# Kernel tuning notes

Measured on AMD Instinct MI355X. Metric: run time of the kernel, lower is better.

## Reference

```python
import jax, jax.numpy as jnp
import numpy as np

B, T, E, H = 4, 1024, 1024, 16
HS = E // H  # 64
EPS = 1e-5


def layernorm(x, g, b):
    mu = jnp.mean(x, axis=-1, keepdims=True)
    var = jnp.mean((x - mu) ** 2, axis=-1, keepdims=True)
    return (x - mu) * jax.lax.rsqrt(var + EPS) * g + b


def setup_inputs() -> dict:
    key = jax.random.key(0)
    ks = jax.random.split(key, 10)
    s = 0.02
    return {
        "v": jax.random.normal(ks[0], (B, T, E), jnp.float32),
        "k": jax.random.normal(ks[1], (B, T, E), jnp.float32),
        "q": jax.random.normal(ks[2], (B, T, E), jnp.float32),
        "ln_g": jnp.ones((E,), jnp.float32),
        "ln_b": jnp.zeros((E,), jnp.float32),
        # per-head projection weights stacked: [E, H, HS] (x @ W form)
        "Wq": jax.random.normal(ks[3], (E, H, HS), jnp.float32) * s,
        "Wk": jax.random.normal(ks[4], (E, H, HS), jnp.float32) * s,
        "Wv": jax.random.normal(ks[5], (E, H, HS), jnp.float32) * s,
        "Wp": jax.random.normal(ks[6], (E, E), jnp.float32) * s,
        "bp": jnp.zeros((E,), jnp.float32),
    }


def reference(v, k, q, ln_g, ln_b, Wq, Wk, Wv, Wp, bp):
    # shared LayerNorm applied to all three streams
    vn = layernorm(v, ln_g, ln_b)
    kn = layernorm(k, ln_g, ln_b)
    qn = layernorm(q, ln_g, ln_b)
    # batched per-head projections: [B,T,E] x [E,H,HS] -> [B,H,T,HS]
    qh = jnp.einsum("bte,ehd->bhtd", qn, Wq)
    kh = jnp.einsum("bte,ehd->bhtd", kn, Wk)
    vh = jnp.einsum("bte,ehd->bhtd", vn, Wv)
    # NOTE: original scales by C^-0.5 where C = embedding_dim (not head_size)
    scale = jnp.float32(E) ** -0.5
    scores = jnp.einsum("bhtd,bhsd->bhts", qh, kh) * scale  # [B,H,T,T]
    causal = jnp.tril(jnp.ones((T, T), bool))
    scores = jnp.where(causal, scores, jnp.finfo(scores.dtype).min)
    w = jax.nn.softmax(scores, axis=-1)
    out = jnp.einsum("bhts,bhsd->bhtd", w, vh)  # [B,H,T,HS]
    out = out.transpose(0, 2, 1, 3).reshape(B, T, E)  # concat heads
    return out @ Wp + bp
```

## Files before the change

kernel.cpp:

```cpp
#include <hip/hip_runtime.h>
#include <stdint.h>

#define B_ 4
#define T_ 1024
#define E_ 1024
#define H_ 16
#define HS_ 64
#define BT_ 4096

typedef unsigned short u16;
typedef __attribute__((ext_vector_type(8))) short bf16x8;
typedef __attribute__((ext_vector_type(4))) float f32x4;

__device__ __forceinline__ u16 f2bf(float f) {
    unsigned u = __float_as_uint(f);
    u += 0x7fff + ((u >> 16) & 1);
    return (u16)(u >> 16);
}

__device__ __forceinline__ u16 f2bf_fast(float f) {
    return (u16)((__float_as_uint(f) + 0x8000u) >> 16);
}

__device__ __forceinline__ float fexp2(float x) {
#if __has_builtin(__builtin_amdgcn_exp2f)
    return __builtin_amdgcn_exp2f(x);
#else
    float r; asm("v_exp_f32 %0, %1" : "=v"(r) : "v"(x)); return r;
#endif
}

__device__ __forceinline__ float frcp(float x) {
#if __has_builtin(__builtin_amdgcn_rcpf)
    return __builtin_amdgcn_rcpf(x);
#else
    float r; asm("v_rcp_f32 %0, %1" : "=v"(r) : "v"(x)); return r;
#endif
}

__device__ __forceinline__ void gll16(const void* g, void* l) {
    __builtin_amdgcn_global_load_lds(
        (const __attribute__((address_space(1))) unsigned int*)g,
        (__attribute__((address_space(3))) unsigned int*)l, 16, 0, 0);
}

__global__ __launch_bounds__(256) void ln_all(
    const float* __restrict__ v, const float* __restrict__ k,
    const float* __restrict__ q, const float* __restrict__ g,
    const float* __restrict__ b,
    u16* __restrict__ vn, u16* __restrict__ kn, u16* __restrict__ qn)
{
    int row = blockIdx.x;
    int which = row >> 12;
    int r = row & 4095;
    const float* src = which == 0 ? v : which == 1 ? k : q;
    u16* dst = which == 0 ? vn : which == 1 ? kn : qn;

    int t = threadIdx.x;
    float4 x = ((const float4*)(src + (size_t)r * E_))[t];
    float s  = x.x + x.y + x.z + x.w;
    float ss = x.x * x.x + x.y * x.y + x.z * x.z + x.w * x.w;
    for (int off = 32; off; off >>= 1) {
        s  += __shfl_down(s, off, 64);
        ss += __shfl_down(ss, off, 64);
    }
    __shared__ float red[8];
    int w = t >> 6, l = t & 63;
    if (l == 0) { red[w] = s; red[4 + w] = ss; }
    __syncthreads();
    float fs  = red[0] + red[1] + red[2] + red[3];
    float fss = red[4] + red[5] + red[6] + red[7];
    float mu  = fs * (1.0f / E_);
    float var = fss * (1.0f / E_) - mu * mu;
    float rstd = rsqrtf(var + 1e-5f);

    float4 gg = ((const float4*)g)[t];
    float4 bb = ((const float4*)b)[t];
    ushort4 o;
    o.x = f2bf((x.x - mu) * rstd * gg.x + bb.x);
    o.y = f2bf((x.y - mu) * rstd * gg.y + bb.y);
    o.z = f2bf((x.z - mu) * rstd * gg.z + bb.z);
    o.w = f2bf((x.w - mu) * rstd * gg.w + bb.w);
    ((ushort4*)(dst + (size_t)r * E_))[t] = o;
}

__global__ __launch_bounds__(256) void wcast_t(
    const float* __restrict__ wq, const float* __restrict__ wk,
    const float* __restrict__ wv, const float* __restrict__ wp,
    u16* __restrict__ tq, u16* __restrict__ tk,
    u16* __restrict__ tv, u16* __restrict__ tp)
{
    int z = blockIdx.z;
    const float* src = z == 0 ? wq : z == 1 ? wk : z == 2 ? wv : wp;
    u16* dst = z == 0 ? tq : z == 1 ? tk : z == 2 ? tv : tp;
    __shared__ float tile[32][33];
    int n0 = blockIdx.x * 32, k0 = blockIdx.y * 32;
    int tx = threadIdx.x & 31, ty = threadIdx.x >> 5;
    for (int i = 0; i < 4; i++)
        tile[ty + i * 8][tx] = src[(size_t)(k0 + ty + i * 8) * E_ + n0 + tx];
    __syncthreads();
    for (int i = 0; i < 4; i++)
        dst[(size_t)(n0 + ty + i * 8) * E_ + k0 + tx] = f2bf(tile[tx][ty + i * 8]);
}

__global__ __launch_bounds__(512, 2) void gemm8ph(
    const u16* __restrict__ Xall, const u16* __restrict__ Wall,
    u16* __restrict__ qh, u16* __restrict__ kh, u16* __restrict__ vt)
{
    __shared__ __attribute__((aligned(16))) u16 lds[2][2][256 * 64];

    int lid = blockIdx.x + 4 * blockIdx.y;
    int swz = (lid & 7) * 24 + (lid >> 3);
    int bx = swz & 3, by = swz >> 2;
    int z  = by >> 4;

    int t = threadIdx.x, w = t >> 6, l = t & 63;
    int lr = l & 15, lg = l >> 4;
    int wm = w >> 2, wn = w & 3;
    int ris = l >> 3;
    int csw = (l & 7) ^ ris;
    int swk = lr & 7;

    const char* Xb = (const char*)Xall + (size_t)by * 256 * 2048;
    const char* Wb = (const char*)Wall + ((size_t)z * 1024 + (size_t)bx * 256) * 2048;

    f32x4 acc[8][4];
    f32x4 zero = {0.f, 0.f, 0.f, 0.f};
    #pragma unroll
    for (int i = 0; i < 8; i++)
        #pragma unroll
        for (int j = 0; j < 4; j++) acc[i][j] = zero;

    auto stage = [&](int kt, int g, int buf) {
        int s = w * 4 + g;
        size_t rowoff = (size_t)(s * 8 + ris) * 2048;
        int koff = kt * 128 + csw * 16;
        gll16(Xb + rowoff + koff, (char*)&lds[buf][0][s * 512] + l * 16);
        gll16(Wb + rowoff + koff, (char*)&lds[buf][1][s * 512] + l * 16);
    };

    for (int g = 0; g < 4; g++) stage(0, g, 0);

    const int NT = 16;
    for (int kt = 0; kt < NT; kt++) {
        int cur = kt & 1, nxt = cur ^ 1;
        bool pre = (kt + 1 < NT);

        if (pre) {
            stage(kt + 1, 0, nxt);
            asm volatile("s_waitcnt vmcnt(2)" ::: "memory");
        } else {
            asm volatile("s_waitcnt vmcnt(0)" ::: "memory");
        }
        __builtin_amdgcn_s_barrier();
        asm volatile("" ::: "memory");

        const u16* As = &lds[cur][0][0];
        const u16* Bs = &lds[cur][1][0];

        bf16x8 bfr[4][2];
        #pragma unroll
        for (int nf = 0; nf < 4; nf++)
            #pragma unroll
            for (int kk = 0; kk < 2; kk++)
                bfr[nf][kk] = *(const bf16x8*)
                    &Bs[(wn * 64 + nf * 16 + lr) * 64 + ((kk * 4 + lg) ^ swk) * 8];

        #pragma unroll
        for (int g = 0; g < 4; g++) {
            if (g && pre) stage(kt + 1, g, nxt);
            bf16x8 af[2][2];
            #pragma unroll
            for (int i = 0; i < 2; i++)
                #pragma unroll
                for (int kk = 0; kk < 2; kk++)
                    af[i][kk] = *(const bf16x8*)
                        &As[(wm * 128 + (g * 2 + i) * 16 + lr) * 64 +
                            ((kk * 4 + lg) ^ swk) * 8];
            __builtin_amdgcn_s_setprio(1);
            #pragma unroll
            for (int i = 0; i < 2; i++)
                #pragma unroll
                for (int nf = 0; nf < 4; nf++)
                    #pragma unroll
                    for (int kk = 0; kk < 2; kk++)
                        acc[g * 2 + i][nf] = __builtin_amdgcn_mfma_f32_16x16x32_bf16(
                            af[i][kk], bfr[nf][kk], acc[g * 2 + i][nf], 0, 0, 0);
            __builtin_amdgcn_s_setprio(0);
        }
        asm volatile("" ::: "memory");
        __builtin_amdgcn_s_barrier();
    }

    if (z < 2) {
        u16* outB = z == 0 ? qh : kh;
        float sc = z == 0 ? 0.04508422f : 1.0f;
        #pragma unroll
        for (int mg = 0; mg < 8; mg++)
            #pragma unroll
            for (int nf = 0; nf < 4; nf++)
                #pragma unroll
                for (int r = 0; r < 4; r++) {
                    int mrow = (by & 15) * 256 + wm * 128 + mg * 16 + lg * 4 + r;
                    int col  = bx * 256 + wn * 64 + nf * 16 + lr;
                    int bb = mrow >> 10, tt = mrow & 1023;
                    int hh = col >> 6, dd = col & 63;
                    outB[(((size_t)(bb * H_ + hh)) * T_ + tt) * HS_ + dd] =
                        f2bf(acc[mg][nf][r] * sc);
                }
    } else {
        __syncthreads();
        u16* Tt = &lds[0][0][0] + w * 4608;
        int hh = bx * 4 + wn;
        u16* outV = vt + ((size_t)(((by & 15) * 256 + wm * 128) >> 10) * H_ + hh)
                         * HS_ * T_;
        #pragma unroll
        for (int half = 0; half < 2; half++) {
            #pragma unroll
            for (int mg2 = 0; mg2 < 4; mg2++)
                #pragma unroll
                for (int nf = 0; nf < 4; nf++)
                    #pragma unroll
                    for (int r = 0; r < 4; r++)
                        Tt[(nf * 16 + lr) * 72 + mg2 * 16 + lg * 4 + r] =
                            f2bf(acc[half * 4 + mg2][nf][r]);
            int mbase = (by & 15) * 256 + wm * 128 + half * 64;
            int tbase = mbase & 1023;
            int dl = l >> 3, tc = l & 7;
            #pragma unroll
            for (int u = 0; u < 8; u++) {
                int d = u * 8 + dl;
                bf16x8 vv = *(const bf16x8*)&Tt[d * 72 + tc * 8];
                *(bf16x8*)&outV[(size_t)d * T_ + tbase + tc * 8] = vv;
            }
        }
    }
}

__global__ __launch_bounds__(256) void gemm128(
    const u16* __restrict__ X, const u16* __restrict__ Wt,
    float* __restrict__ outF, const float* __restrict__ bias)
{
    __shared__ __attribute__((aligned(16))) char smem[32768];
    int lid = blockIdx.x + 8 * blockIdx.y;
    int swz = (lid & 7) * 32 + (lid >> 3);
    int bx = swz & 7;
    int by = swz >> 3;

    const int K = 1024;
    int n0 = bx * 128, m0 = by * 128;
    int t = threadIdx.x, w = t >> 6, l = t & 63;
    int lr = l & 15, lg = l >> 4, wm = w >> 1, wn = w & 1;

    f32x4 acc[4][4];
    f32x4 zero = {0.f, 0.f, 0.f, 0.f};
    for (int i = 0; i < 4; i++)
        for (int j = 0; j < 4; j++) acc[i][j] = zero;

    const char* Xb = (const char*)X + (size_t)m0 * 2048;
    const char* Wb = (const char*)Wt + (size_t)n0 * 2048;

    int scol = ((l & 3) ^ ((l >> 3) & 3)) * 16;

    auto stage = [&](int k0, int buf) {
        int kb = k0 * 2;
        for (int j = 0; j < 2; j++) {
            int seg = w * 2 + j;
            int row = seg * 16 + (l >> 2);
            gll16(Xb + (size_t)row * 2048 + kb + scol,
                  smem + buf * 8192 + seg * 1024 + l * 16);
            gll16(Wb + (size_t)row * 2048 + kb + scol,
                  smem + 16384 + buf * 8192 + seg * 1024 + l * 16);
        }
    };

    stage(0, 0);
    __syncthreads();
    int b = 0;
    int swr = (lr >> 1) & 3;
    for (int k0 = 0; k0 < K; k0 += 32) {
        if (k0 + 32 < K) stage(k0 + 32, b ^ 1);
        const u16* As = (const u16*)(smem + b * 8192);
        const u16* Bs = (const u16*)(smem + 16384 + b * 8192);
        bf16x8 af[4], bfr[4];
        for (int i = 0; i < 4; i++)
            af[i] = *(const bf16x8*)&As[(wm * 64 + i * 16 + lr) * 32 + (lg ^ swr) * 8];
        for (int j = 0; j < 4; j++)
            bfr[j] = *(const bf16x8*)&Bs[(wn * 64 + j * 16 + lr) * 32 + (lg ^ swr) * 8];
        for (int i = 0; i < 4; i++)
            for (int j = 0; j < 4; j++)
                acc[i][j] = __builtin_amdgcn_mfma_f32_16x16x32_bf16(
                    af[i], bfr[j], acc[i][j], 0, 0, 0);
        __syncthreads();
        b ^= 1;
    }

    for (int i = 0; i < 4; i++)
        for (int j = 0; j < 4; j++)
            for (int r = 0; r < 4; r++) {
                int row = m0 + wm * 64 + i * 16 + lg * 4 + r;
                int col = n0 + wn * 64 + j * 16 + lr;
                outF[(size_t)row * E_ + col] = acc[i][j][r] + bias[col];
            }
}

__global__ __launch_bounds__(256) void attn(
    const u16* __restrict__ Qh, const u16* __restrict__ Kh,
    const u16* __restrict__ Vt, u16* __restrict__ Out)
{
    int lid = blockIdx.x + 8 * blockIdx.y;
    int swz = (lid & 7) * 64 + (lid >> 3);
    int qt = 7 - (swz & 7);
    int bh = swz >> 3;
    int b = bh >> 4, h = bh & 15;
    int t = threadIdx.x, w = t >> 6, l = t & 63;
    int lr = l & 15, lg = l >> 4;
    int sw = lr & 7;

    __shared__ __attribute__((aligned(16))) u16 Ks[2][4096];
    __shared__ __attribute__((aligned(16))) u16 Vs[2][4096];
    __shared__ __attribute__((aligned(16))) u16 Ps[4][2048];

    const char* Kb = (const char*)(Kh + (size_t)bh * T_ * HS_);
    const char* Vb = (const char*)(Vt + (size_t)bh * HS_ * T_);
    const u16*  Qb = Qh + (size_t)bh * T_ * HS_;

    int ris = l >> 3;
    int csw = (l & 7) ^ ris;

    bf16x8 qf[2][2];
    for (int i = 0; i < 2; i++) {
        int qrow = qt * 128 + w * 32 + i * 16 + lr;
        qf[i][0] = *(const bf16x8*)&Qb[qrow * 64 + lg * 8];
        qf[i][1] = *(const bf16x8*)&Qb[qrow * 64 + 32 + lg * 8];
    }

    f32x4 zero = {0.f, 0.f, 0.f, 0.f};
    f32x4 o[2][4];
    float m[2][4], psum[2][4];
    for (int i = 0; i < 2; i++)
        for (int nf = 0; nf < 4; nf++) o[i][nf] = zero;
    for (int i = 0; i < 2; i++)
        for (int r = 0; r < 4; r++) { m[i][r] = -1e30f; psum[i][r] = 0.f; }

    int nkv = 2 * qt + 2;

    auto stageKV = [&](int kt2, int bsel) {
        int kv0 = kt2 * 64;
        for (int j = 0; j < 2; j++) {
            int seg = w * 2 + j;
            int row = seg * 8 + ris;
            gll16(Kb + (size_t)(kv0 + row) * 128 + csw * 16,
                  (char*)Ks[bsel] + seg * 1024);
            gll16(Vb + (size_t)row * 2048 + (size_t)kv0 * 2 + csw * 16,
                  (char*)Vs[bsel] + seg * 1024);
        }
    };

    stageKV(0, 0);
    __syncthreads();
    int bsel = 0;

    for (int kt = 0; kt < nkv; kt++) {
        if (kt + 1 < nkv) stageKV(kt + 1, bsel ^ 1);

        int kv0 = kt * 64;
        const u16* Kl = Ks[bsel];
        const u16* Vl = Vs[bsel];

        f32x4 s[2][4];
        __builtin_amdgcn_s_setprio(1);
        for (int kf = 0; kf < 4; kf++) {
            int key = kf * 16 + lr;
            bf16x8 bk0 = *(const bf16x8*)&Kl[key * 64 + (lg ^ sw) * 8];
            bf16x8 bk1 = *(const bf16x8*)&Kl[key * 64 + ((lg + 4) ^ sw) * 8];
            for (int i = 0; i < 2; i++) {
                s[i][kf] = __builtin_amdgcn_mfma_f32_16x16x32_bf16(qf[i][0], bk0, zero, 0, 0, 0);
                s[i][kf] = __builtin_amdgcn_mfma_f32_16x16x32_bf16(qf[i][1], bk1, s[i][kf], 0, 0, 0);
            }
        }
        __builtin_amdgcn_s_setprio(0);

        if (kt >= 2 * qt) {
            for (int i = 0; i < 2; i++)
                for (int kf = 0; kf < 4; kf++)
                    for (int r = 0; r < 4; r++) {
                        int key = kv0 + kf * 16 + lr;
                        int qr  = qt * 128 + w * 32 + i * 16 + lg * 4 + r;
                        if (key > qr) s[i][kf][r] = -1e30f;
                    }
        }

        float pmr[2][4];
        bool ok = true;
        for (int i = 0; i < 2; i++)
            for (int r = 0; r < 4; r++) {
                pmr[i][r] = fmaxf(fmaxf(s[i][0][r], s[i][1][r]),
                                  fmaxf(s[i][2][r], s[i][3][r]));
                ok &= (pmr[i][r] <= m[i][r] + 11.5f);
            }
        if (!__all(ok)) {
            for (int i = 0; i < 2; i++)
                for (int r = 0; r < 4; r++) {
                    float mt = pmr[i][r];
                    for (int off = 1; off < 16; off <<= 1)
                        mt = fmaxf(mt, __shfl_xor(mt, off, 64));
                    float mn = fmaxf(m[i][r], mt);
                    float al = fexp2(m[i][r] - mn);
                    m[i][r] = mn;
                    psum[i][r] *= al;
                    for (int nf = 0; nf < 4; nf++) o[i][nf][r] *= al;
                }
        }

        for (int i = 0; i < 2; i++)
            for (int kf = 0; kf < 4; kf++)
                for (int r = 0; r < 4; r++) {
                    float p = fexp2(s[i][kf][r] - m[i][r]);
                    psum[i][r] += p;
                    int row = i * 16 + lg * 4 + r;
                    int ch  = (kf * 2 + (lr >> 3)) ^ (row & 7);
                    Ps[w][row * 64 + ch * 8 + sw] = f2bf_fast(p);
                }

        __builtin_amdgcn_s_setprio(1);
        for (int ks = 0; ks < 2; ks++) {
            bf16x8 pa0 = *(const bf16x8*)&Ps[w][(lr) * 64 + ((ks * 4 + lg) ^ sw) * 8];
            bf16x8 pa1 = *(const bf16x8*)&Ps[w][(16 + lr) * 64 + ((ks * 4 + lg) ^ sw) * 8];
            for (int nf = 0; nf < 4; nf++) {
                int d = nf * 16 + lr;
                bf16x8 bv = *(const bf16x8*)&Vl[d * 64 + ((ks * 4 + lg) ^ sw) * 8];
                o[0][nf] = __builtin_amdgcn_mfma_f32_16x16x32_bf16(pa0, bv, o[0][nf], 0, 0, 0);
                o[1][nf] = __builtin_amdgcn_mfma_f32_16x16x32_bf16(pa1, bv, o[1][nf], 0, 0, 0);
            }
        }
        __builtin_amdgcn_s_setprio(0);
        __syncthreads();
        bsel ^= 1;
    }

    for (int i = 0; i < 2; i++)
        for (int r = 0; r < 4; r++) {
            for (int off = 1; off < 16; off <<= 1)
                psum[i][r] += __shfl_xor(psum[i][r], off, 64);
            psum[i][r] = frcp(psum[i][r]);
        }

    for (int i = 0; i < 2; i++)
        for (int nf = 0; nf < 4; nf++)
            for (int r = 0; r < 4; r++) {
                int row = qt * 128 + w * 32 + i * 16 + lg * 4 + r;
                int col = h * 64 + nf * 16 + lr;
                Out[((size_t)(b * T_ + row)) * E_ + col] = f2bf(o[i][nf][r] * psum[i][r]);
            }
}

extern "C" void kernel_launch(void* const* d_in, const int* in_sizes, int n_in,
                              void* d_out, int out_size, void* d_ws, size_t ws_size,
                              hipStream_t stream) {
    const float* v  = (const float*)d_in[0];
    const float* k  = (const float*)d_in[1];
    const float* q  = (const float*)d_in[2];
    const float* g  = (const float*)d_in[3];
    const float* be = (const float*)d_in[4];
    const float* Wq = (const float*)d_in[5];
    const float* Wk = (const float*)d_in[6];
    const float* Wv = (const float*)d_in[7];
    const float* Wp = (const float*)d_in[8];
    const float* bp = (const float*)d_in[9];
    float* out = (float*)d_out;

    char* ws = (char*)d_ws;
    u16* qh  = (u16*)(ws);
    u16* kh  = (u16*)(ws + (8u  << 20));
    u16* vt  = (u16*)(ws + (16u << 20));
    u16* qn  = (u16*)(ws + (24u << 20));
    u16* kn  = (u16*)(ws + (32u << 20));
    u16* vn  = (u16*)(ws + (40u << 20));
    u16* wtq = (u16*)(ws + (48u << 20));
    u16* wtk = (u16*)(ws + (50u << 20));
    u16* wtv = (u16*)(ws + (52u << 20));
    u16* wtp = (u16*)(ws + (54u << 20));
    u16* ao  = (u16*)(ws + (24u << 20));

    hipLaunchKernelGGL(wcast_t, dim3(32, 32, 4), dim3(256), 0, stream,
                       Wq, Wk, Wv, Wp, wtq, wtk, wtv, wtp);
    hipLaunchKernelGGL(ln_all, dim3(3 * BT_), dim3(256), 0, stream,
                       v, k, q, g, be, vn, kn, qn);
    hipLaunchKernelGGL(gemm8ph, dim3(4, 48), dim3(512), 0, stream,
                       qn, wtq, qh, kh, vt);
    hipLaunchKernelGGL(attn, dim3(8, 64), dim3(256), 0, stream,
                       qh, kh, vt, ao);
    hipLaunchKernelGGL(gemm128, dim3(8, 32), dim3(256), 0, stream,
                       ao, wtp, out, bp);
}
```

Before: 202.8 us.

## Split attention tile across 8 waves and compute row sums via MFMA

The attention kernel now launches 512 threads (8 waves) per 128-query block, with each wave owning 16 query rows instead of 32. This halves per-wave registers and gives more waves to hide latency. The softmax denominator is now computed with an extra MFMA against a ones vector using the bf16-rounded probabilities, which replaces the scalar psum accumulation and the final cross-lane shuffle reduction. In exchange, each wave makes fewer MFMAs per LDS load of K and V fragments, and the per-block shared-memory staging is split across more waves.

Measured after the change: 198.2 us. 2.3% less time.

```diff
diff --git a/kernel.cpp b/kernel.cpp
--- a/kernel.cpp
+++ b/kernel.cpp
@@ -304,7 +304,7 @@
             }
 }
 
-__global__ __launch_bounds__(256) void attn(
+__global__ __launch_bounds__(512, 4) void attn(
     const u16* __restrict__ Qh, const u16* __restrict__ Kh,
     const u16* __restrict__ Vt, u16* __restrict__ Out)
 {
@@ -319,7 +319,7 @@
 
     __shared__ __attribute__((aligned(16))) u16 Ks[2][4096];
     __shared__ __attribute__((aligned(16))) u16 Vs[2][4096];
-    __shared__ __attribute__((aligned(16))) u16 Ps[4][2048];
+    __shared__ __attribute__((aligned(16))) u16 Ps[8][1024];
 
     const char* Kb = (const char*)(Kh + (size_t)bh * T_ * HS_);
     const char* Vb = (const char*)(Vt + (size_t)bh * HS_ * T_);
@@ -328,33 +328,30 @@
     int ris = l >> 3;
     int csw = (l & 7) ^ ris;
 
-    bf16x8 qf[2][2];
-    for (int i = 0; i < 2; i++) {
-        int qrow = qt * 128 + w * 32 + i * 16 + lr;
-        qf[i][0] = *(const bf16x8*)&Qb[qrow * 64 + lg * 8];
-        qf[i][1] = *(const bf16x8*)&Qb[qrow * 64 + 32 + lg * 8];
-    }
+    int qrow = qt * 128 + w * 16 + lr;
+    bf16x8 qf0 = *(const bf16x8*)&Qb[qrow * 64 + lg * 8];
+    bf16x8 qf1 = *(const bf16x8*)&Qb[qrow * 64 + 32 + lg * 8];
+
+    bf16x8 onesb;
+    #pragma unroll
+    for (int j = 0; j < 8; j++) onesb[j] = (short)0x3F80;
 
     f32x4 zero = {0.f, 0.f, 0.f, 0.f};
-    f32x4 o[2][4];
-    float m[2][4], psum[2][4];
-    for (int i = 0; i < 2; i++)
-        for (int nf = 0; nf < 4; nf++) o[i][nf] = zero;
-    for (int i = 0; i < 2; i++)
-        for (int r = 0; r < 4; r++) { m[i][r] = -1e30f; psum[i][r] = 0.f; }
+    f32x4 o[4], ps;
+    float m[4];
+    for (int nf = 0; nf < 4; nf++) o[nf] = zero;
+    ps = zero;
+    for (int r = 0; r < 4; r++) m[r] = -1e30f;
 
     int nkv = 2 * qt + 2;
 
     auto stageKV = [&](int kt2, int bsel) {
         int kv0 = kt2 * 64;
-        for (int j = 0; j < 2; j++) {
-            int seg = w * 2 + j;
-            int row = seg * 8 + ris;
-            gll16(Kb + (size_t)(kv0 + row) * 128 + csw * 16,
-                  (char*)Ks[bsel] + seg * 1024);
-            gll16(Vb + (size_t)row * 2048 + (size_t)kv0 * 2 + csw * 16,
-                  (char*)Vs[bsel] + seg * 1024);
-        }
+        int row = w * 8 + ris;
+        gll16(Kb + (size_t)(kv0 + row) * 128 + csw * 16,
+              (char*)Ks[bsel] + w * 1024);
+        gll16(Vb + (size_t)row * 2048 + (size_t)kv0 * 2 + csw * 16,
+              (char*)Vs[bsel] + w * 1024);
     };
 
     stageKV(0, 0);
@@ -368,70 +365,61 @@
         const u16* Kl = Ks[bsel];
         const u16* Vl = Vs[bsel];
 
-        f32x4 s[2][4];
+        f32x4 s[4];
         __builtin_amdgcn_s_setprio(1);
         for (int kf = 0; kf < 4; kf++) {
             int key = kf * 16 + lr;
             bf16x8 bk0 = *(const bf16x8*)&Kl[key * 64 + (lg ^ sw) * 8];
             bf16x8 bk1 = *(const bf16x8*)&Kl[key * 64 + ((lg + 4) ^ sw) * 8];
-            for (int i = 0; i < 2; i++) {
-                s[i][kf] = __builtin_amdgcn_mfma_f32_16x16x32_bf16(qf[i][0], bk0, zero, 0, 0, 0);
-                s[i][kf] = __builtin_amdgcn_mfma_f32_16x16x32_bf16(qf[i][1], bk1, s[i][kf], 0, 0, 0);
-            }
+            s[kf] = __builtin_amdgcn_mfma_f32_16x16x32_bf16(qf0, bk0, zero, 0, 0, 0);
+            s[kf] = __builtin_amdgcn_mfma_f32_16x16x32_bf16(qf1, bk1, s[kf], 0, 0, 0);
         }
         __builtin_amdgcn_s_setprio(0);
 
         if (kt >= 2 * qt) {
-            for (int i = 0; i < 2; i++)
-                for (int kf = 0; kf < 4; kf++)
-                    for (int r = 0; r < 4; r++) {
-                        int key = kv0 + kf * 16 + lr;
-                        int qr  = qt * 128 + w * 32 + i * 16 + lg * 4 + r;
-                        if (key > qr) s[i][kf][r] = -1e30f;
-                    }
-        }
-
-        float pmr[2][4];
-        bool ok = true;
-        for (int i = 0; i < 2; i++)
-            for (int r = 0; r < 4; r++) {
-                pmr[i][r] = fmaxf(fmaxf(s[i][0][r], s[i][1][r]),
-                                  fmaxf(s[i][2][r], s[i][3][r]));
-                ok &= (pmr[i][r] <= m[i][r] + 11.5f);
-            }
-        if (!__all(ok)) {
-            for (int i = 0; i < 2; i++)
-                for (int r = 0; r < 4; r++) {
-                    float mt = pmr[i][r];
-                    for (int off = 1; off < 16; off <<= 1)
-                        mt = fmaxf(mt, __shfl_xor(mt, off, 64));
-                    float mn = fmaxf(m[i][r], mt);
-                    float al = fexp2(m[i][r] - mn);
-                    m[i][r] = mn;
-                    psum[i][r] *= al;
-                    for (int nf = 0; nf < 4; nf++) o[i][nf][r] *= al;
-                }
-        }
-
-        for (int i = 0; i < 2; i++)
             for (int kf = 0; kf < 4; kf++)
                 for (int r = 0; r < 4; r++) {
-                    float p = fexp2(s[i][kf][r] - m[i][r]);
-                    psum[i][r] += p;
-                    int row = i * 16 + lg * 4 + r;
-                    int ch  = (kf * 2 + (lr >> 3)) ^ (row & 7);
-                    Ps[w][row * 64 + ch * 8 + sw] = f2bf_fast(p);
+                    int key = kv0 + kf * 16 + lr;
+                    int qr  = qt * 128 + w * 16 + lg * 4 + r;
+                    if (key > qr) s[kf][r] = -1e30f;
                 }
+        }
+
+        float pmr[4];
+        bool ok = true;
+        for (int r = 0; r < 4; r++) {
+            pmr[r] = fmaxf(fmaxf(s[0][r], s[1][r]), fmaxf(s[2][r], s[3][r]));
+            ok &= (pmr[r] <= m[r] + 11.5f);
+        }
+        if (!__all(ok)) {
+            for (int r = 0; r < 4; r++) {
+                float mt = pmr[r];
+                for (int off = 1; off < 16; off <<= 1)
+                    mt = fmaxf(mt, __shfl_xor(mt, off, 64));
+                float mn = fmaxf(m[r], mt);
+                float al = fexp2(m[r] - mn);
+                m[r] = mn;
+                ps[r] *= al;
+                for (int nf = 0; nf < 4; nf++) o[nf][r] *= al;
+            }
+        }
+
+        for (int kf = 0; kf < 4; kf++)
+            for (int r = 0; r < 4; r++) {
+                float p = fexp2(s[kf][r] - m[r]);
+                int row = lg * 4 + r;
+                int ch  = (kf * 2 + (lr >> 3)) ^ (row & 7);
+                Ps[w][row * 64 + ch * 8 + sw] = f2bf_fast(p);
+            }
 
         __builtin_amdgcn_s_setprio(1);
         for (int ks = 0; ks < 2; ks++) {
-            bf16x8 pa0 = *(const bf16x8*)&Ps[w][(lr) * 64 + ((ks * 4 + lg) ^ sw) * 8];
-            bf16x8 pa1 = *(const bf16x8*)&Ps[w][(16 + lr) * 64 + ((ks * 4 + lg) ^ sw) * 8];
+            bf16x8 pa = *(const bf16x8*)&Ps[w][lr * 64 + ((ks * 4 + lg) ^ sw) * 8];
+            ps = __builtin_amdgcn_mfma_f32_16x16x32_bf16(pa, onesb, ps, 0, 0, 0);
             for (int nf = 0; nf < 4; nf++) {
                 int d = nf * 16 + lr;
                 bf16x8 bv = *(const bf16x8*)&Vl[d * 64 + ((ks * 4 + lg) ^ sw) * 8];
-                o[0][nf] = __builtin_amdgcn_mfma_f32_16x16x32_bf16(pa0, bv, o[0][nf], 0, 0, 0);
-                o[1][nf] = __builtin_amdgcn_mfma_f32_16x16x32_bf16(pa1, bv, o[1][nf], 0, 0, 0);
+                o[nf] = __builtin_amdgcn_mfma_f32_16x16x32_bf16(pa, bv, o[nf], 0, 0, 0);
             }
         }
         __builtin_amdgcn_s_setprio(0);
@@ -439,20 +427,15 @@
         bsel ^= 1;
     }
 
-    for (int i = 0; i < 2; i++)
+    float rs[4];
+    for (int r = 0; r < 4; r++) rs[r] = frcp(ps[r]);
+
+    for (int nf = 0; nf < 4; nf++)
         for (int r = 0; r < 4; r++) {
-            for (int off = 1; off < 16; off <<= 1)
-                psum[i][r] += __shfl_xor(psum[i][r], off, 64);
-            psum[i][r] = frcp(psum[i][r]);
-        }
-
-    for (int i = 0; i < 2; i++)
-        for (int nf = 0; nf < 4; nf++)
-            for (int r = 0; r < 4; r++) {
-                int row = qt * 128 + w * 32 + i * 16 + lg * 4 + r;
-                int col = h * 64 + nf * 16 + lr;
-                Out[((size_t)(b * T_ + row)) * E_ + col] = f2bf(o[i][nf][r] * psum[i][r]);
-            }
+            int row = qt * 128 + w * 16 + lg * 4 + r;
+            int col = h * 64 + nf * 16 + lr;
+            Out[((size_t)(b * T_ + row)) * E_ + col] = f2bf(o[nf][r] * rs[r]);
+        }
 }
 
 extern "C" void kernel_launch(void* const* d_in, const int* in_sizes, int n_in,
@@ -489,7 +472,7 @@
                        v, k, q, g, be, vn, kn, qn);
     hipLaunchKernelGGL(gemm8ph, dim3(4, 48), dim3(512), 0, stream,
                        qn, wtq, qh, kh, vt);
-    hipLaunchKernelGGL(attn, dim3(8, 64), dim3(256), 0, stream,
+    hipLaunchKernelGGL(attn, dim3(8, 64), dim3(512), 0, stream,
                        qh, kh, vt, ao);
     hipLaunchKernelGGL(gemm128, dim3(8, 32), dim3(256), 0, stream,
                        ao, wtp, out, bp);
```
